# Kernel optimization log

Measured on AMD Instinct MI355X. Metric: run time of the kernel, lower is better.

Reference implementation:

```python
import jax, jax.numpy as jnp
import numpy as np

E, S, D, A, L, H, C = 8, 6000, 128, 16, 64, 256, 64
B = 50            # no_batches hardcoded in torch forward
T = S // B        # number of outer integration steps
DT = 0.5          # solver dt; t_horizon=[0,1] -> 2 reversible-Heun substeps
NSUB = 2
SQDT = float(np.sqrt(DT))


def setup_inputs():
    ks = jax.random.split(jax.random.key(0), 24)
    w = lambda k, shp, s=0.05: (jax.random.normal(k, shp) * s).astype(jnp.float32)
    z = lambda shp: jnp.zeros(shp, jnp.float32)
    return dict(
        xs=w(ks[0], (E, S, D), 1.0),
        actions=w(ks[1], (E, S, A), 1.0),
        z0_noise=w(ks[2], (T, E, B, L), 1.0),
        dW=w(ks[3], (T, NSUB, E * B, L), 1.0),
        enc_w1=w(ks[4], (E, D, H)), enc_b1=z((E, H)),
        enc_w2=w(ks[5], (E, H, C)), enc_b2=z((E, C)),
        qz0_w=w(ks[6], (E, C, 2 * L)), qz0_b=z((E, 2 * L)),
        act_w=w(ks[7], (E, L + A + D, L)), act_b=z((E, L)),
        fw1=w(ks[8], (L, H)), fb1=z((H,)),
        fw2=w(ks[9], (H, H)), fb2=z((H,)),
        fw3=w(ks[10], (H, L)), fb3=z((L,)),
        hw1=w(ks[11], (L, H)), hb1=z((H,)),
        hw2=w(ks[12], (H, H)), hb2=z((H,)),
        hw3=w(ks[13], (H, L)), hb3=z((L,)),
        gw1=w(ks[14], (L, H)), gb1=z((L, H)),
        gw2=w(ks[15], (L, H), 0.02), gb2=jnp.ones((L,), jnp.float32),
        pw1=w(ks[16], (E, L, H)), pb1=z((E, H)),
        pw2=w(ks[17], (E, H, H)), pb2=z((E, H)),
        pw3=w(ks[18], (E, H, D)), pb3=z((E, D)),
        pz0_mean=z((E, 1, L)), pz0_logstd=z((E, 1, L)),
    )


def reference(xs, actions, z0_noise, dW,
              enc_w1, enc_b1, enc_w2, enc_b2, qz0_w, qz0_b, act_w, act_b,
              fw1, fb1, fw2, fb2, fw3, fb3, hw1, hb1, hw2, hb2, hw3, hb3,
              gw1, gb1, gw2, gb2, pw1, pb1, pw2, pb2, pw3, pb3,
              pz0_mean, pz0_logstd):
    xs_r = xs.reshape(E, T, B, D).transpose(1, 0, 2, 3)       # [T,E,B,D]
    act_r = actions.reshape(E, T, B, A).transpose(1, 0, 2, 3)  # [T,E,B,A]

    def mlp3(y, w1, b1, w2, b2, w3, b3):
        h1 = jax.nn.sigmoid(y @ w1 + b1)
        h2 = jax.nn.sigmoid(h1 @ w2 + b2)
        return h2 @ w3 + b3

    def g_fn(y):  # per-latent-dim diagonal diffusion nets, vectorized over L
        hc = jax.nn.sigmoid(y[..., None] * gw1 + gb1)          # [N,L,H]
        return jnp.sum(hc * gw2, axis=-1) + gb2                # [N,L]

    def drift_all(zc):
        fz = mlp3(zc, fw1, fb1, fw2, fb2, fw3, fb3)
        hz = mlp3(zc, hw1, hb1, hw2, hb2, hw3, hb3)
        gz = g_fn(zc)
        u = (fz - hz) / gz
        return fz, gz, 0.5 * jnp.sum(u * u, axis=-1)           # logqp drift

    def sde_solve(zini, dWs):  # reversible Heun, Stratonovich, logqp-augmented
        zc = zh = zini
        lc = lh = jnp.zeros(zini.shape[0], zini.dtype)
        fz, gz, lf = drift_all(zc)
        for k in range(NSUB):
            dWk = dWs[k] * SQDT
            zh_n = 2.0 * zc - zh + fz * DT + gz * dWk
            lh_n = 2.0 * lc - lh + lf * DT
            fz1, gz1, lf1 = drift_all(zh_n)
            zc = zc + 0.5 * (fz + fz1) * DT + 0.5 * (gz + gz1) * dWk
            lc = lc + 0.5 * (lf + lf1) * DT
            zh, lh, fz, gz, lf = zh_n, lh_n, fz1, gz1, lf1
        return zc, lc

    def step(z_prev, inp):
        i, x_i, a_i, n_i, dW_i = inp
        c1 = jax.nn.sigmoid(jnp.einsum('ebd,edh->ebh', x_i, enc_w1) + enc_b1[:, None])
        ctx = jnp.einsum('ebh,ehc->ebc', c1, enc_w2) + enc_b2[:, None]
        q = jnp.einsum('ebc,eck->ebk', ctx, qz0_w) + qz0_b[:, None]
        qm, ql = q[..., :L], q[..., L:]
        z0 = qm + jnp.exp(ql) * n_i
        z_in = jnp.where(i == 0, z0, z_prev)
        lat = jnp.concatenate([z_in, a_i, x_i], axis=-1)
        z_enc = jnp.einsum('ebf,efl->ebl', lat, act_w) + act_b[:, None]
        zf, lr = sde_solve(z_enc.reshape(E * B, L), dW_i)
        z_new = zf.reshape(E, B, L)
        p1 = jax.nn.sigmoid(jnp.einsum('ebl,elh->ebh', z_new, pw1) + pb1[:, None])
        p2 = jax.nn.sigmoid(jnp.einsum('ebh,ehk->ebk', p1, pw2) + pb2[:, None])
        xm = jnp.einsum('ebh,ehd->ebd', p2, pw3) + pb3[:, None]
        # KL(q(z0) || p(z0)) elementwise, p has mean pz0_mean, logstd pz0_logstd
        kl = (pz0_logstd - ql
              + (jnp.exp(2.0 * ql) + (qm - pz0_mean) ** 2) / (2.0 * jnp.exp(2.0 * pz0_logstd))
              - 0.5)
        logqp0 = kl.sum(-1).mean(-1)  # [E]
        return z_new, (xm, lr.reshape(E, B), logqp0)

    z_init = jnp.zeros((E, B, L), xs.dtype)
    _, (xm_all, lr_all, lq0_all) = jax.lax.scan(
        step, z_init, (jnp.arange(T), xs_r, act_r, z0_noise, dW))
    predicted_xs = xm_all.transpose(1, 0, 2, 3).reshape(E, T * B, D)
    logqp_path = lr_all.mean(-1).sum(0) + lq0_all.sum(0)  # [E]
    return logqp_path, predicted_xs
```

## Files before the change

kernel.cpp:

```cpp
#include <hip/hip_runtime.h>
#include <math.h>

#define E 8
#define S 6000
#define D 128
#define A 16
#define L 64
#define H 256
#define C 64
#define B 50
#define T 120
#define NSUB 2
#define FLAT 208
#define RTOT 400
#define RPB 10
#define NBLK (RTOT / RPB)
#define BGRP 10
#define NBG 5

#define DT 0.5f
#define SQDT 0.70710678118654752440f

#define GNT 4096
#define GYMIN (-128.0f)
#define GDY 0.0625f
#define GINVDY 16.0f

typedef __attribute__((ext_vector_type(8))) short bf16x8;
typedef __attribute__((ext_vector_type(4))) float f32x4;

#define MFMA16(a, b, c) __builtin_amdgcn_mfma_f32_16x16x32_bf16(a, b, c, 0, 0, 0)

__device__ __forceinline__ float sigf(float x) {
    return __builtin_amdgcn_rcpf(1.0f + __expf(-x));
}

__device__ __forceinline__ unsigned short f2bf(float x) {
    union { float f; unsigned u; } v; v.f = x;
    return (unsigned short)((v.u + 0x8000u) >> 16);
}

__device__ __forceinline__ void bar_lgkm() {
    asm volatile("s_waitcnt lgkmcnt(0)" ::: "memory");
    __builtin_amdgcn_s_barrier();
}

__global__ void gtab_kernel(const float* __restrict__ gw1, const float* __restrict__ gb1,
                            const float* __restrict__ gw2, const float* __restrict__ gb2,
                            float* __restrict__ tab) {
    int idx = blockIdx.x * blockDim.x + threadIdx.x;
    if (idx >= L * GNT) return;
    int l = idx / GNT, i = idx % GNT;
    float y = GYMIN + (float)i * GDY;
    const float* w1 = gw1 + l * H;
    const float* b1 = gb1 + l * H;
    const float* w2 = gw2 + l * H;
    float acc = gb2[l];
    #pragma unroll 4
    for (int h = 0; h < H; ++h) acc += w2[h] * (1.0f / (1.0f + __expf(-(y * w1[h] + b1[h]))));
    tab[idx] = acc;
}

__global__ void packB_kernel(const float* __restrict__ src, unsigned short* __restrict__ dst,
                             int K, int N) {
    int idx = blockIdx.x * 256 + threadIdx.x;
    if (idx >= K * N) return;
    int j = idx & 7;
    int lane = (idx >> 3) & 63;
    int t2 = idx >> 9;
    int KC = K >> 5;
    int kc = t2 % KC, n = t2 / KC;
    int k = (kc << 5) + ((lane >> 4) << 3) + j;
    int c = (n << 4) + (lane & 15);
    union { float f; unsigned u; } v; v.f = src[k * N + c];
    dst[idx] = (unsigned short)((v.u + 0x7FFFu + ((v.u >> 16) & 1u)) >> 16);
}

__global__ void packAW_kernel(const float* __restrict__ aw, unsigned short* __restrict__ dst) {
    int idx = blockIdx.x * 256 + threadIdx.x;
    if (idx >= E * L * L) return;
    int e = idx >> 12;
    int rem = idx & 4095;
    int j = rem & 7;
    int lane = (rem >> 3) & 63;
    int t2 = rem >> 9;
    int kc = t2 & 1, n = t2 >> 1;
    int k = (kc << 5) + ((lane >> 4) << 3) + j;
    int c = (n << 4) + (lane & 15);
    union { float f; unsigned u; } v; v.f = aw[((size_t)e * FLAT + k) * L + c];
    dst[idx] = (unsigned short)((v.u + 0x7FFFu + ((v.u >> 16) & 1u)) >> 16);
}

__global__ __launch_bounds__(256) void enc_kernel(const float* __restrict__ xs, const float* __restrict__ z0n,
                           const float* __restrict__ ew1, const float* __restrict__ eb1,
                           const float* __restrict__ ew2, const float* __restrict__ eb2,
                           const float* __restrict__ qw,  const float* __restrict__ qb,
                           const float* __restrict__ pm,  const float* __restrict__ pl,
                           float* __restrict__ z0buf, float* __restrict__ logqp0p) {
    int bid = blockIdx.x;
    int bg = bid % NBG; int te = bid / NBG; int e = te % E; int t = te / E;
    int tid = threadIdx.x;
    __shared__ float xsh[BGRP][D];
    __shared__ float c1s[BGRP][H];
    __shared__ float part[4][C][BGRP];
    __shared__ float ctxs[BGRP][C];
    __shared__ float qs[BGRP][2 * L];

    for (int i = tid; i < BGRP * D; i += 256) {
        int j = i / D, d = i % D;
        xsh[j][d] = xs[((size_t)e * S + (size_t)t * B + bg * BGRP + j) * D + d];
    }
    __syncthreads();
    {
        float bias = eb1[e * H + tid];
        float acc[BGRP];
        #pragma unroll
        for (int j = 0; j < BGRP; ++j) acc[j] = bias;
        const float* w = ew1 + (size_t)e * D * H + tid;
        #pragma unroll 4
        for (int d = 0; d < D; ++d) {
            float wv = w[(size_t)d * H];
            #pragma unroll
            for (int j = 0; j < BGRP; ++j) acc[j] += xsh[j][d] * wv;
        }
        #pragma unroll
        for (int j = 0; j < BGRP; ++j) c1s[j][tid] = sigf(acc[j]);
    }
    __syncthreads();
    {
        int c = tid & 63, kq = tid >> 6;
        float acc[BGRP];
        #pragma unroll
        for (int j = 0; j < BGRP; ++j) acc[j] = 0.f;
        const float* w = ew2 + (size_t)e * H * C + c;
        #pragma unroll 4
        for (int h = kq * 64; h < kq * 64 + 64; ++h) {
            float wv = w[(size_t)h * C];
            #pragma unroll
            for (int j = 0; j < BGRP; ++j) acc[j] += c1s[j][h] * wv;
        }
        #pragma unroll
        for (int j = 0; j < BGRP; ++j) part[kq][c][j] = acc[j];
    }
    __syncthreads();
    if (tid < C) {
        float bias = eb2[e * C + tid];
        #pragma unroll
        for (int j = 0; j < BGRP; ++j)
            ctxs[j][tid] = part[0][tid][j] + part[1][tid][j] + part[2][tid][j] + part[3][tid][j] + bias;
    }
    __syncthreads();
    if (tid < 2 * L) {
        float bias = qb[e * 2 * L + tid];
        float acc[BGRP];
        #pragma unroll
        for (int j = 0; j < BGRP; ++j) acc[j] = bias;
        const float* w = qw + (size_t)e * C * 2 * L + tid;
        #pragma unroll 4
        for (int c = 0; c < C; ++c) {
            float wv = w[(size_t)c * 2 * L];
            #pragma unroll
            for (int j = 0; j < BGRP; ++j) acc[j] += ctxs[j][c] * wv;
        }
        #pragma unroll
        for (int j = 0; j < BGRP; ++j) qs[j][tid] = acc[j];
    }
    __syncthreads();
    if (tid < L) {
        int l = tid;
        float kacc = 0.f;
        float m = pm[e * L + l], ls = pl[e * L + l];
        float inv2e = 1.0f / (2.0f * __expf(2.0f * ls));
        #pragma unroll
        for (int j = 0; j < BGRP; ++j) {
            float qm = qs[j][l], ql = qs[j][L + l];
            if (t == 0) {
                int b = bg * BGRP + j;
                float n = z0n[((size_t)e * B + b) * L + l];
                z0buf[((size_t)e * B + b) * L + l] = qm + __expf(ql) * n;
            }
            float dq = qm - m;
            kacc += ls - ql + (__expf(2.f * ql) + dq * dq) * inv2e - 0.5f;
        }
        #pragma unroll
        for (int off = 32; off; off >>= 1) kacc += __shfl_xor(kacc, off);
        if (l == 0) logqp0p[bid] = kacc / (float)B;
    }
}

__global__ __launch_bounds__(64) void ax_kernel(const float* __restrict__ xs, const float* __restrict__ actions,
                          const float* __restrict__ aw, const float* __restrict__ ab,
                          float* __restrict__ ax) {
    int bid = blockIdx.x;
    int bg = bid % NBG; int te = bid / NBG; int e = te % E; int t = te / E;
    int tid = threadIdx.x;
    __shared__ float xrow[BGRP][D];
    __shared__ float arow[BGRP][A];
    for (int i = tid; i < BGRP * D; i += 64) {
        int j = i / D, d = i % D;
        xrow[j][d] = xs[((size_t)e * S + (size_t)t * B + bg * BGRP + j) * D + d];
    }
    for (int i = tid; i < BGRP * A; i += 64) {
        int j = i / A, a = i % A;
        arow[j][a] = actions[((size_t)e * S + (size_t)t * B + bg * BGRP + j) * A + a];
    }
    __syncthreads();
    int l = tid;
    float acc[BGRP];
    float bias = ab[e * L + l];
    #pragma unroll
    for (int j = 0; j < BGRP; ++j) acc[j] = bias;
    const float* awp = aw + ((size_t)e * FLAT + L) * L + l;
    #pragma unroll 4
    for (int a = 0; a < A; ++a) {
        float wv = awp[(size_t)a * L];
        #pragma unroll
        for (int j = 0; j < BGRP; ++j) acc[j] += arow[j][a] * wv;
    }
    const float* xwp = aw + ((size_t)e * FLAT + L + A) * L + l;
    #pragma unroll 4
    for (int d = 0; d < D; ++d) {
        float wv = xwp[(size_t)d * L];
        #pragma unroll
        for (int j = 0; j < BGRP; ++j) acc[j] += xrow[j][d] * wv;
    }
    size_t rbase = (size_t)t * RTOT + e * B + bg * BGRP;
    #pragma unroll
    for (int j = 0; j < BGRP; ++j) ax[(rbase + j) * L + l] = acc[j];
}

__global__ __launch_bounds__(512, 2) void seq_kernel(
    const unsigned short* __restrict__ pkAW, const float* __restrict__ dW,
    const float* __restrict__ z0buf, const float* __restrict__ axbuf,
    const unsigned short* __restrict__ pk1, const unsigned short* __restrict__ pk2,
    const unsigned short* __restrict__ pk3,
    const float* __restrict__ fb1, const float* __restrict__ hb1,
    const float* __restrict__ fb2, const float* __restrict__ hb2,
    const float* __restrict__ fb3, const float* __restrict__ hb3,
    const float* __restrict__ gtab, float* __restrict__ z_all, float* __restrict__ rowlr)
{
    __shared__ __align__(16) bf16x8 w1L[4096];
    __shared__ __align__(16) unsigned short ybfA[1024];
    __shared__ __align__(16) unsigned short ybfZ[1024];
    __shared__ __align__(16) unsigned short o1[2][4096];
    __shared__ __align__(16) unsigned short o2[2][4096];
    __shared__ float fh2[2][16][64];
    __shared__ float zcS[16][64];
    __shared__ float axS[RPB * L];

    int tid = threadIdx.x;
    int wv = tid >> 6;
    int lane = tid & 63;
    int rA = lane & 15, kg = lane >> 4;
    int sw = (rA & 7) << 3;
    int r_base = blockIdx.x * RPB;
    int e = blockIdx.x / 5;

    for (int i = tid; i < 4096; i += 512) w1L[i] = ((const bf16x8*)pk1)[i];

    int net = wv >> 2;
    int nq  = wv & 3;
    int na  = nq << 2;
    int n0c = nq;
    int lZ = (nq << 4) + rA;

    bf16x8 W0r0 = {}, W0r1 = {}, W2r[32], W3r[8];
    if (wv < 4) {
        const bf16x8* p0 = (const bf16x8*)pkAW + (e << 9);
        W0r0 = p0[(nq * 2 + 0) * 64 + lane];
        W0r1 = p0[(nq * 2 + 1) * 64 + lane];
    }
    {
        const bf16x8* p2 = (const bf16x8*)pk2 + net * 8192;
        #pragma unroll
        for (int i2 = 0; i2 < 4; ++i2)
            #pragma unroll
            for (int kc = 0; kc < 8; ++kc)
                W2r[i2 * 8 + kc] = p2[((na + i2) * 8 + kc) * 64 + lane];
        const bf16x8* p3 = (const bf16x8*)pk3 + net * 2048;
        #pragma unroll
        for (int kc = 0; kc < 8; ++kc)
            W3r[kc] = p3[(n0c * 8 + kc) * 64 + lane];
    }
    float biasA[4], biasB[4], biasC;
    {
        const float* b1 = net ? hb1 : fb1;
        const float* b2 = net ? hb2 : fb2;
        const float* b3 = net ? hb3 : fb3;
        #pragma unroll
        for (int i2 = 0; i2 < 4; ++i2) {
            biasA[i2] = b1[((na + i2) << 4) + rA];
            biasB[i2] = b2[((na + i2) << 4) + rA];
        }
        biasC = b3[(n0c << 4) + rA];
    }

    int orowA = tid >> 6, olA = tid & 63;
    bool ownB = (tid < RPB * L - 512);
    int orowB = 8 + (tid >> 6);
    float zcA = 0.f, zhA_ = 0.f, fzA = 0.f, gzA = 1.f, dwAA = 0.f, dwBA = 0.f;
    float gtA0 = 1.f, gtA1 = 1.f, gfrA = 0.f, scalA = 0.f;
    float zcB = 0.f, zhB_ = 0.f, fzB = 0.f, gzB = 1.f, dwAB = 0.f, dwBB = 0.f;
    float gtB0 = 1.f, gtB1 = 1.f, gfrB = 0.f, scalB = 0.f;

    for (int i = tid; i < 1024; i += 512) {
        int r = i >> 6;
        float v = (i < RPB * L) ? z0buf[(size_t)r_base * L + i] : 0.f;
        ybfZ[i ^ ((r & 7) << 3)] = f2bf(v);
    }
    axS[tid] = axbuf[((size_t)0 * RTOT + r_base) * L + tid];
    if (ownB) axS[512 + tid] = axbuf[((size_t)0 * RTOT + r_base) * L + 512 + tid];
    __syncthreads();

    auto gprepA = [&](float v) {
        float x = (v - GYMIN) * GINVDY;
        x = fminf(fmaxf(x, 0.0f), (float)(GNT - 2) + 0.999f);
        int ii = (int)x;
        gfrA = x - (float)ii;
        const float* tl = gtab + ((size_t)olA << 12);
        gtA0 = tl[ii];
        gtA1 = tl[ii + 1];
    };
    auto gprepB = [&](float v) {
        float x = (v - GYMIN) * GINVDY;
        x = fminf(fmaxf(x, 0.0f), (float)(GNT - 2) + 0.999f);
        int ii = (int)x;
        gfrB = x - (float)ii;
        const float* tl = gtab + ((size_t)olA << 12);
        gtB0 = tl[ii];
        gtB1 = tl[ii + 1];
    };

    for (int t = 0; t < T; ++t) {
        if (wv < 4) {
            bf16x8 Z0 = *(const bf16x8*)&ybfZ[((rA << 6) + (kg << 3)) ^ sw];
            bf16x8 Z1 = *(const bf16x8*)&ybfZ[((rA << 6) + 32 + (kg << 3)) ^ sw];
            f32x4 acc = (f32x4){0.f, 0.f, 0.f, 0.f};
            acc = MFMA16(Z0, W0r0, acc);
            acc = MFMA16(Z1, W0r1, acc);
            #pragma unroll
            for (int rr = 0; rr < 4; ++rr) {
                int r = (kg << 2) + rr;
                float axv = (r < RPB) ? axS[(r << 6) + lZ] : 0.f;
                float v = acc[rr] + axv;
                zcS[r][lZ] = v;
                ybfA[((r << 6) + lZ) ^ ((r & 7) << 3)] = f2bf(v);
            }
        }
        bar_lgkm();

        #pragma clang loop unroll(disable)
        for (int d = 0; d < 3; ++d) {
            if (d == 0) {
                zcA = zcS[orowA][olA];
                zhA_ = zcA;
                gprepA(zcA);
                dwAA = dW[((size_t)(2 * t) * RTOT + r_base) * L + tid] * SQDT;
                dwBA = dW[((size_t)(2 * t + 1) * RTOT + r_base) * L + tid] * SQDT;
                int tn = (t + 1 < T) ? t + 1 : t;
                axS[tid] = axbuf[((size_t)tn * RTOT + r_base) * L + tid];
                if (ownB) {
                    zcB = zcS[orowB][olA];
                    zhB_ = zcB;
                    gprepB(zcB);
                    dwAB = dW[((size_t)(2 * t) * RTOT + r_base) * L + 512 + tid] * SQDT;
                    dwBB = dW[((size_t)(2 * t + 1) * RTOT + r_base) * L + 512 + tid] * SQDT;
                    axS[512 + tid] = axbuf[((size_t)tn * RTOT + r_base) * L + 512 + tid];
                }
            }
            {
                bf16x8 A0 = *(const bf16x8*)&ybfA[((rA << 6) + (kg << 3)) ^ sw];
                bf16x8 A1 = *(const bf16x8*)&ybfA[((rA << 6) + 32 + (kg << 3)) ^ sw];
                f32x4 acc[4];
                #pragma unroll
                for (int i2 = 0; i2 < 4; ++i2) {
                    acc[i2] = (f32x4){biasA[i2], biasA[i2], biasA[i2], biasA[i2]};
                    acc[i2] = MFMA16(A0, w1L[net * 2048 + ((na + i2) * 2 + 0) * 64 + lane], acc[i2]);
                    acc[i2] = MFMA16(A1, w1L[net * 2048 + ((na + i2) * 2 + 1) * 64 + lane], acc[i2]);
                }
                unsigned short* o1n = o1[net];
                #pragma unroll
                for (int i2 = 0; i2 < 4; ++i2) {
                    int c = ((na + i2) << 4) + rA;
                    #pragma unroll
                    for (int rr = 0; rr < 4; ++rr) {
                        int r = (kg << 2) + rr;
                        o1n[((r << 8) + c) ^ ((r & 7) << 3)] = f2bf(sigf(acc[i2][rr]));
                    }
                }
            }
            bar_lgkm();
            {
                const unsigned short* o1n = o1[net];
                f32x4 acc[4];
                #pragma unroll
                for (int i2 = 0; i2 < 4; ++i2)
                    acc[i2] = (f32x4){biasB[i2], biasB[i2], biasB[i2], biasB[i2]};
                #pragma unroll
                for (int kc = 0; kc < 8; ++kc) {
                    bf16x8 Ak = *(const bf16x8*)&o1n[((rA << 8) + (kc << 5) + (kg << 3)) ^ sw];
                    #pragma unroll
                    for (int i2 = 0; i2 < 4; ++i2)
                        acc[i2] = MFMA16(Ak, W2r[i2 * 8 + kc], acc[i2]);
                }
                unsigned short* o2n = o2[net];
                #pragma unroll
                for (int i2 = 0; i2 < 4; ++i2) {
                    int c = ((na + i2) << 4) + rA;
                    #pragma unroll
                    for (int rr = 0; rr < 4; ++rr) {
                        int r = (kg << 2) + rr;
                        o2n[((r << 8) + c) ^ ((r & 7) << 3)] = f2bf(sigf(acc[i2][rr]));
                    }
                }
            }
            bar_lgkm();
            {
                const unsigned short* o2n = o2[net];
                f32x4 acc = (f32x4){biasC, biasC, biasC, biasC};
                f32x4 accb = (f32x4){0.f, 0.f, 0.f, 0.f};
                #pragma unroll
                for (int kc = 0; kc < 4; ++kc) {
                    bf16x8 Ak0 = *(const bf16x8*)&o2n[((rA << 8) + ((2 * kc) << 5) + (kg << 3)) ^ sw];
                    bf16x8 Ak1 = *(const bf16x8*)&o2n[((rA << 8) + ((2 * kc + 1) << 5) + (kg << 3)) ^ sw];
                    acc  = MFMA16(Ak0, W3r[2 * kc], acc);
                    accb = MFMA16(Ak1, W3r[2 * kc + 1], accb);
                }
                int c = (n0c << 4) + rA;
                #pragma unroll
                for (int rr = 0; rr < 4; ++rr)
                    fh2[net][(kg << 2) + rr][c] = acc[rr] + accb[rr];
            }
            bar_lgkm();
            {
                float fvA = fh2[0][orowA][olA];
                float hvA = fh2[1][orowA][olA];
                float gvA = gtA0 * (1.0f - gfrA) + gtA1 * gfrA;
                float uA = (fvA - hvA) / gvA;
                float usA = uA * uA;
                float fvB = 0.f, hvB = 0.f, gvB = 1.f, usB = 0.f;
                if (ownB) {
                    fvB = fh2[0][orowB][olA];
                    hvB = fh2[1][orowB][olA];
                    gvB = gtB0 * (1.0f - gfrB) + gtB1 * gfrB;
                    float uB = (fvB - hvB) / gvB;
                    usB = uB * uB;
                }
                if (d == 0) {
                    scalA += usA; fzA = fvA; gzA = gvA;
                    float y1 = zcA + fvA * DT + gvA * dwAA;
                    zhA_ = y1;
                    ybfA[tid ^ ((orowA & 7) << 3)] = f2bf(y1);
                    gprepA(y1);
                    if (ownB) {
                        scalB += usB; fzB = fvB; gzB = gvB;
                        float y1b = zcB + fvB * DT + gvB * dwAB;
                        zhB_ = y1b;
                        ybfA[(512 + tid) ^ ((orowB & 7) << 3)] = f2bf(y1b);
                        gprepB(y1b);
                    }
                } else if (d == 1) {
                    zcA += 0.5f * (fzA + fvA) * DT + 0.5f * (gzA + gvA) * dwAA;
                    scalA += 2.0f * usA;
                    float y2 = 2.f * zcA - zhA_ + fvA * DT + gvA * dwBA;
                    fzA = fvA; gzA = gvA;
                    ybfA[tid ^ ((orowA & 7) << 3)] = f2bf(y2);
                    gprepA(y2);
                    if (ownB) {
                        zcB += 0.5f * (fzB + fvB) * DT + 0.5f * (gzB + gvB) * dwAB;
                        scalB += 2.0f * usB;
                        float y2b = 2.f * zcB - zhB_ + fvB * DT + gvB * dwBB;
                        fzB = fvB; gzB = gvB;
                        ybfA[(512 + tid) ^ ((orowB & 7) << 3)] = f2bf(y2b);
                        gprepB(y2b);
                    }
                } else {
                    zcA += 0.5f * (fzA + fvA) * DT + 0.5f * (gzA + gvA) * dwBA;
                    scalA += usA;
                    z_all[((size_t)t * RTOT + r_base) * L + tid] = zcA;
                    ybfZ[tid ^ ((orowA & 7) << 3)] = f2bf(zcA);
                    if (ownB) {
                        zcB += 0.5f * (fzB + fvB) * DT + 0.5f * (gzB + gvB) * dwBB;
                        scalB += usB;
                        z_all[((size_t)t * RTOT + r_base) * L + 512 + tid] = zcB;
                        ybfZ[(512 + tid) ^ ((orowB & 7) << 3)] = f2bf(zcB);
                    }
                }
            }
            bar_lgkm();
        }
    }
    {
        float s = scalA;
        #pragma unroll
        for (int off = 32; off; off >>= 1) s += __shfl_xor(s, off);
        if (olA == 0) rowlr[r_base + orowA] = 0.25f * DT * s;
        float sb = ownB ? scalB : 0.f;
        #pragma unroll
        for (int off = 32; off; off >>= 1) sb += __shfl_xor(sb, off);
        if (ownB && olA == 0) rowlr[r_base + orowB] = 0.25f * DT * sb;
    }
}

__global__ __launch_bounds__(256) void proj_kernel(const float* __restrict__ z_all,
                            const float* __restrict__ pw1, const float* __restrict__ pb1,
                            const float* __restrict__ pw2, const float* __restrict__ pb2,
                            const float* __restrict__ pw3, const float* __restrict__ pb3,
                            float* __restrict__ out) {
    int bid = blockIdx.x;
    int bg = bid % NBG; int te = bid / NBG; int e = te % E; int t = te / E;
    int tid = threadIdx.x;
    __shared__ float zs[BGRP][L];
    __shared__ float p1s[BGRP][H];
    __shared__ float p2s[BGRP][H];
    __shared__ float part3[D][BGRP];
    size_t rbase = (size_t)t * RTOT + e * B + bg * BGRP;
    for (int i = tid; i < BGRP * L; i += 256) {
        int j = i >> 6, ll = i & 63;
        zs[j][ll] = z_all[(rbase + j) * L + ll];
    }
    __syncthreads();
    {
        float bias = pb1[e * H + tid];
        float acc[BGRP];
        #pragma unroll
        for (int j = 0; j < BGRP; ++j) acc[j] = bias;
        const float* w = pw1 + (size_t)e * L * H + tid;
        #pragma unroll 4
        for (int k = 0; k < L; ++k) {
            float wv = w[(size_t)k * H];
            #pragma unroll
            for (int j = 0; j < BGRP; ++j) acc[j] += zs[j][k] * wv;
        }
        #pragma unroll
        for (int j = 0; j < BGRP; ++j) p1s[j][tid] = sigf(acc[j]);
    }
    __syncthreads();
    {
        float bias = pb2[e * H + tid];
        float acc[BGRP];
        #pragma unroll
        for (int j = 0; j < BGRP; ++j) acc[j] = bias;
        const float* w = pw2 + (size_t)e * H * H + tid;
        #pragma unroll 4
        for (int k = 0; k < H; ++k) {
            float wv = w[(size_t)k * H];
            #pragma unroll
            for (int j = 0; j < BGRP; ++j) acc[j] += p1s[j][k] * wv;
        }
        #pragma unroll
        for (int j = 0; j < BGRP; ++j) p2s[j][tid] = sigf(acc[j]);
    }
    __syncthreads();
    float acc3[BGRP];
    {
        int dd = tid & 127, kh = tid >> 7;
        #pragma unroll
        for (int j = 0; j < BGRP; ++j) acc3[j] = 0.f;
        const float* w = pw3 + (size_t)e * H * D + dd;
        #pragma unroll 4
        for (int k = kh * 128; k < kh * 128 + 128; ++k) {
            float wv = w[(size_t)k * D];
            #pragma unroll
            for (int j = 0; j < BGRP; ++j) acc3[j] += p2s[j][k] * wv;
        }
        if (kh == 1) {
            #pragma unroll
            for (int j = 0; j < BGRP; ++j) part3[dd][j] = acc3[j];
        }
    }
    __syncthreads();
    if (tid < D) {
        float bias = pb3[e * D + tid];
        #pragma unroll
        for (int j = 0; j < BGRP; ++j) {
            out[8 + ((size_t)e * S + (size_t)t * B + bg * BGRP + j) * D + tid]
                = acc3[j] + part3[tid][j] + bias;
        }
    }
}

__global__ void fin_kernel(const float* __restrict__ logqp0p, const float* __restrict__ rowlr,
                           float* __restrict__ out) {
    int e = threadIdx.x;
    if (e < E) {
        float acc = 0.f;
        for (int t = 0; t < T; ++t)
            for (int bg = 0; bg < NBG; ++bg)
                acc += logqp0p[(t * E + e) * NBG + bg];
        float s = 0.f;
        for (int b = 0; b < B; ++b) s += rowlr[e * B + b];
        out[e] = acc + s / (float)B;
    }
}

extern "C" void kernel_launch(void* const* d_in, const int* in_sizes, int n_in,
                              void* d_out, int out_size, void* d_ws, size_t ws_size,
                              hipStream_t stream) {
    const float* xs      = (const float*)d_in[0];
    const float* actions = (const float*)d_in[1];
    const float* z0n     = (const float*)d_in[2];
    const float* dWp     = (const float*)d_in[3];
    const float* ew1     = (const float*)d_in[4];
    const float* eb1     = (const float*)d_in[5];
    const float* ew2     = (const float*)d_in[6];
    const float* eb2     = (const float*)d_in[7];
    const float* qw      = (const float*)d_in[8];
    const float* qb      = (const float*)d_in[9];
    const float* aw      = (const float*)d_in[10];
    const float* ab      = (const float*)d_in[11];
    const float* fw1     = (const float*)d_in[12];
    const float* fb1     = (const float*)d_in[13];
    const float* fw2     = (const float*)d_in[14];
    const float* fb2     = (const float*)d_in[15];
    const float* fw3     = (const float*)d_in[16];
    const float* fb3     = (const float*)d_in[17];
    const float* hw1     = (const float*)d_in[18];
    const float* hb1     = (const float*)d_in[19];
    const float* hw2     = (const float*)d_in[20];
    const float* hb2     = (const float*)d_in[21];
    const float* hw3     = (const float*)d_in[22];
    const float* hb3     = (const float*)d_in[23];
    const float* gw1     = (const float*)d_in[24];
    const float* gb1     = (const float*)d_in[25];
    const float* gw2     = (const float*)d_in[26];
    const float* gb2     = (const float*)d_in[27];
    const float* pw1     = (const float*)d_in[28];
    const float* pb1     = (const float*)d_in[29];
    const float* pw2     = (const float*)d_in[30];
    const float* pb2     = (const float*)d_in[31];
    const float* pw3     = (const float*)d_in[32];
    const float* pb3     = (const float*)d_in[33];
    const float* pm      = (const float*)d_in[34];
    const float* pl      = (const float*)d_in[35];

    float* ws      = (float*)d_ws;
    float* z0buf   = ws;
    float* axbuf   = z0buf + 25600;
    float* z_all   = axbuf + 3072000;
    float* logqp0p = z_all + 3072000;
    float* rowlr   = logqp0p + 4800;
    float* gtab    = rowlr + 400;
    unsigned short* pku = (unsigned short*)(gtab + 262144);
    unsigned short* pk1 = pku;
    unsigned short* pk2 = pk1 + 32768;
    unsigned short* pk3 = pk2 + 131072;
    unsigned short* pkAW = pk3 + 32768;
    float* out     = (float*)d_out;

    packB_kernel<<<64,  256, 0, stream>>>(fw1, pk1,          64, 256);
    packB_kernel<<<64,  256, 0, stream>>>(hw1, pk1 + 16384,  64, 256);
    packB_kernel<<<256, 256, 0, stream>>>(fw2, pk2,          256, 256);
    packB_kernel<<<256, 256, 0, stream>>>(hw2, pk2 + 65536,  256, 256);
    packB_kernel<<<64,  256, 0, stream>>>(fw3, pk3,          256, 64);
    packB_kernel<<<64,  256, 0, stream>>>(hw3, pk3 + 16384,  256, 64);
    packAW_kernel<<<128, 256, 0, stream>>>(aw, pkAW);
    gtab_kernel<<<1024, 256, 0, stream>>>(gw1, gb1, gw2, gb2, gtab);
    enc_kernel<<<T * E * NBG, 256, 0, stream>>>(xs, z0n, ew1, eb1, ew2, eb2, qw, qb, pm, pl, z0buf, logqp0p);
    ax_kernel<<<T * E * NBG, 64, 0, stream>>>(xs, actions, aw, ab, axbuf);
    seq_kernel<<<NBLK, 512, 0, stream>>>(pkAW, dWp, z0buf, axbuf,
                                         pk1, pk2, pk3,
                                         fb1, hb1, fb2, hb2, fb3, hb3,
                                         gtab, z_all, rowlr);
    proj_kernel<<<T * E * NBG, 256, 0, stream>>>(z_all, pw1, pb1, pw2, pb2, pw3, pb3, out);
    fin_kernel<<<1, 64, 0, stream>>>(logqp0p, rowlr, out);
}
```

Measured before the change: 2.617 ms.

## Fuse output MLP layer and SDE update into four waves, dropping a barrier

New measurement: 3.462 ms. 32.3% more time.

```diff
diff --git a/kernel.cpp b/kernel.cpp
--- a/kernel.cpp
+++ b/kernel.cpp
@@ -240,13 +240,13 @@
     const float* __restrict__ gtab, float* __restrict__ z_all, float* __restrict__ rowlr)
 {
     __shared__ __align__(16) bf16x8 w1L[4096];
+    __shared__ __align__(16) bf16x8 w0L[512];
+    __shared__ __align__(16) bf16x8 fw3L[2048];
     __shared__ __align__(16) unsigned short ybfA[1024];
     __shared__ __align__(16) unsigned short ybfZ[1024];
     __shared__ __align__(16) unsigned short o1[2][4096];
     __shared__ __align__(16) unsigned short o2[2][4096];
-    __shared__ float fh2[2][16][64];
-    __shared__ float zcS[16][64];
-    __shared__ float axS[RPB * L];
+    __shared__ float scalS[16][64];
 
     int tid = threadIdx.x;
     int wv = tid >> 6;
@@ -257,19 +257,14 @@
     int e = blockIdx.x / 5;
 
     for (int i = tid; i < 4096; i += 512) w1L[i] = ((const bf16x8*)pk1)[i];
+    w0L[tid] = ((const bf16x8*)pkAW)[(e << 9) + tid];
+    for (int i = tid; i < 2048; i += 512) fw3L[i] = ((const bf16x8*)pk3)[i];
 
     int net = wv >> 2;
     int nq  = wv & 3;
     int na  = nq << 2;
-    int n0c = nq;
-    int lZ = (nq << 4) + rA;
-
-    bf16x8 W0r0 = {}, W0r1 = {}, W2r[32], W3r[8];
-    if (wv < 4) {
-        const bf16x8* p0 = (const bf16x8*)pkAW + (e << 9);
-        W0r0 = p0[(nq * 2 + 0) * 64 + lane];
-        W0r1 = p0[(nq * 2 + 1) * 64 + lane];
-    }
+
+    bf16x8 W2r[32], hW3r[8];
     {
         const bf16x8* p2 = (const bf16x8*)pk2 + net * 8192;
         #pragma unroll
@@ -277,97 +272,63 @@
             #pragma unroll
             for (int kc = 0; kc < 8; ++kc)
                 W2r[i2 * 8 + kc] = p2[((na + i2) * 8 + kc) * 64 + lane];
-        const bf16x8* p3 = (const bf16x8*)pk3 + net * 2048;
+        const bf16x8* p3h = (const bf16x8*)pk3 + 2048;
         #pragma unroll
         for (int kc = 0; kc < 8; ++kc)
-            W3r[kc] = p3[(n0c * 8 + kc) * 64 + lane];
-    }
-    float biasA[4], biasB[4], biasC;
+            hW3r[kc] = p3h[(nq * 8 + kc) * 64 + lane];
+    }
+    float biasA[4], biasB[4];
     {
         const float* b1 = net ? hb1 : fb1;
         const float* b2 = net ? hb2 : fb2;
-        const float* b3 = net ? hb3 : fb3;
         #pragma unroll
         for (int i2 = 0; i2 < 4; ++i2) {
             biasA[i2] = b1[((na + i2) << 4) + rA];
             biasB[i2] = b2[((na + i2) << 4) + rA];
         }
-        biasC = b3[(n0c << 4) + rA];
-    }
-
-    int orowA = tid >> 6, olA = tid & 63;
-    bool ownB = (tid < RPB * L - 512);
-    int orowB = 8 + (tid >> 6);
-    float zcA = 0.f, zhA_ = 0.f, fzA = 0.f, gzA = 1.f, dwAA = 0.f, dwBA = 0.f;
-    float gtA0 = 1.f, gtA1 = 1.f, gfrA = 0.f, scalA = 0.f;
-    float zcB = 0.f, zhB_ = 0.f, fzB = 0.f, gzB = 1.f, dwAB = 0.f, dwBB = 0.f;
-    float gtB0 = 1.f, gtB1 = 1.f, gfrB = 0.f, scalB = 0.f;
+    }
+    int cc = (nq << 4) + rA;
+    float biasCf = fb3[cc], biasCh = hb3[cc];
+
+    float zc[4], zh[4], fz[4], gz[4], yv[4], scal[4], dwA[4], dwB[4];
+    #pragma unroll
+    for (int i = 0; i < 4; ++i) { zc[i]=0.f; zh[i]=0.f; fz[i]=0.f; gz[i]=1.f; yv[i]=0.f; scal[i]=0.f; dwA[i]=0.f; dwB[i]=0.f; }
 
     for (int i = tid; i < 1024; i += 512) {
         int r = i >> 6;
         float v = (i < RPB * L) ? z0buf[(size_t)r_base * L + i] : 0.f;
         ybfZ[i ^ ((r & 7) << 3)] = f2bf(v);
     }
-    axS[tid] = axbuf[((size_t)0 * RTOT + r_base) * L + tid];
-    if (ownB) axS[512 + tid] = axbuf[((size_t)0 * RTOT + r_base) * L + 512 + tid];
-    __syncthreads();
-
-    auto gprepA = [&](float v) {
-        float x = (v - GYMIN) * GINVDY;
-        x = fminf(fmaxf(x, 0.0f), (float)(GNT - 2) + 0.999f);
-        int ii = (int)x;
-        gfrA = x - (float)ii;
-        const float* tl = gtab + ((size_t)olA << 12);
-        gtA0 = tl[ii];
-        gtA1 = tl[ii + 1];
-    };
-    auto gprepB = [&](float v) {
-        float x = (v - GYMIN) * GINVDY;
-        x = fminf(fmaxf(x, 0.0f), (float)(GNT - 2) + 0.999f);
-        int ii = (int)x;
-        gfrB = x - (float)ii;
-        const float* tl = gtab + ((size_t)olA << 12);
-        gtB0 = tl[ii];
-        gtB1 = tl[ii + 1];
-    };
+    __syncthreads();
 
     for (int t = 0; t < T; ++t) {
         if (wv < 4) {
+            float axv[4];
+            #pragma unroll
+            for (int i = 0; i < 4; ++i) {
+                int r = (kg << 2) + i;
+                bool real = (r < RPB);
+                axv[i] = real ? axbuf[((size_t)t * RTOT + r_base + r) * L + cc] : 0.f;
+                dwA[i] = real ? dW[((size_t)(2 * t) * RTOT + r_base + r) * L + cc] * SQDT : 0.f;
+                dwB[i] = real ? dW[((size_t)(2 * t + 1) * RTOT + r_base + r) * L + cc] * SQDT : 0.f;
+            }
             bf16x8 Z0 = *(const bf16x8*)&ybfZ[((rA << 6) + (kg << 3)) ^ sw];
             bf16x8 Z1 = *(const bf16x8*)&ybfZ[((rA << 6) + 32 + (kg << 3)) ^ sw];
             f32x4 acc = (f32x4){0.f, 0.f, 0.f, 0.f};
-            acc = MFMA16(Z0, W0r0, acc);
-            acc = MFMA16(Z1, W0r1, acc);
-            #pragma unroll
-            for (int rr = 0; rr < 4; ++rr) {
-                int r = (kg << 2) + rr;
-                float axv = (r < RPB) ? axS[(r << 6) + lZ] : 0.f;
-                float v = acc[rr] + axv;
-                zcS[r][lZ] = v;
-                ybfA[((r << 6) + lZ) ^ ((r & 7) << 3)] = f2bf(v);
+            acc = MFMA16(Z0, w0L[(nq * 2 + 0) * 64 + lane], acc);
+            acc = MFMA16(Z1, w0L[(nq * 2 + 1) * 64 + lane], acc);
+            #pragma unroll
+            for (int i = 0; i < 4; ++i) {
+                int r = (kg << 2) + i;
+                float v = acc[i] + axv[i];
+                zc[i] = v; zh[i] = v; yv[i] = v;
+                ybfA[((r << 6) + cc) ^ ((r & 7) << 3)] = f2bf(v);
             }
         }
         bar_lgkm();
 
         #pragma clang loop unroll(disable)
         for (int d = 0; d < 3; ++d) {
-            if (d == 0) {
-                zcA = zcS[orowA][olA];
-                zhA_ = zcA;
-                gprepA(zcA);
-                dwAA = dW[((size_t)(2 * t) * RTOT + r_base) * L + tid] * SQDT;
-                dwBA = dW[((size_t)(2 * t + 1) * RTOT + r_base) * L + tid] * SQDT;
-                int tn = (t + 1 < T) ? t + 1 : t;
-                axS[tid] = axbuf[((size_t)tn * RTOT + r_base) * L + tid];
-                if (ownB) {
-                    zcB = zcS[orowB][olA];
-                    zhB_ = zcB;
-                    gprepB(zcB);
-                    dwAB = dW[((size_t)(2 * t) * RTOT + r_base) * L + 512 + tid] * SQDT;
-                    dwBB = dW[((size_t)(2 * t + 1) * RTOT + r_base) * L + 512 + tid] * SQDT;
-                    axS[512 + tid] = axbuf[((size_t)tn * RTOT + r_base) * L + 512 + tid];
-                }
-            }
             {
                 bf16x8 A0 = *(const bf16x8*)&ybfA[((rA << 6) + (kg << 3)) ^ sw];
                 bf16x8 A1 = *(const bf16x8*)&ybfA[((rA << 6) + 32 + (kg << 3)) ^ sw];
@@ -415,90 +376,79 @@
                 }
             }
             bar_lgkm();
-            {
-                const unsigned short* o2n = o2[net];
-                f32x4 acc = (f32x4){biasC, biasC, biasC, biasC};
-                f32x4 accb = (f32x4){0.f, 0.f, 0.f, 0.f};
+            if (wv < 4) {
+                float gt0[4], gt1[4], gfr[4];
+                const float* tl = gtab + ((size_t)cc << 12);
+                #pragma unroll
+                for (int i = 0; i < 4; ++i) {
+                    float x = (yv[i] - GYMIN) * GINVDY;
+                    x = fminf(fmaxf(x, 0.0f), (float)(GNT - 2) + 0.999f);
+                    int ii = (int)x;
+                    gfr[i] = x - (float)ii;
+                    gt0[i] = tl[ii];
+                    gt1[i] = tl[ii + 1];
+                }
+                const unsigned short* o2f = o2[0];
+                const unsigned short* o2h = o2[1];
+                f32x4 aF = (f32x4){biasCf, biasCf, biasCf, biasCf};
+                f32x4 bF = (f32x4){0.f, 0.f, 0.f, 0.f};
+                f32x4 aH = (f32x4){biasCh, biasCh, biasCh, biasCh};
+                f32x4 bH = (f32x4){0.f, 0.f, 0.f, 0.f};
                 #pragma unroll
                 for (int kc = 0; kc < 4; ++kc) {
-                    bf16x8 Ak0 = *(const bf16x8*)&o2n[((rA << 8) + ((2 * kc) << 5) + (kg << 3)) ^ sw];
-                    bf16x8 Ak1 = *(const bf16x8*)&o2n[((rA << 8) + ((2 * kc + 1) << 5) + (kg << 3)) ^ sw];
-                    acc  = MFMA16(Ak0, W3r[2 * kc], acc);
-                    accb = MFMA16(Ak1, W3r[2 * kc + 1], accb);
+                    bf16x8 Af0 = *(const bf16x8*)&o2f[((rA << 8) + ((2*kc) << 5) + (kg << 3)) ^ sw];
+                    bf16x8 Af1 = *(const bf16x8*)&o2f[((rA << 8) + ((2*kc+1) << 5) + (kg << 3)) ^ sw];
+                    aF = MFMA16(Af0, fw3L[(nq * 8 + 2*kc) * 64 + lane], aF);
+                    bF = MFMA16(Af1, fw3L[(nq * 8 + 2*kc+1) * 64 + lane], bF);
+                    bf16x8 Ah0 = *(const bf16x8*)&o2h[((rA << 8) + ((2*kc) << 5) + (kg << 3)) ^ sw];
+                    bf16x8 Ah1 = *(const bf16x8*)&o2h[((rA << 8) + ((2*kc+1) << 5) + (kg << 3)) ^ sw];
+                    aH = MFMA16(Ah0, hW3r[2*kc], aH);
+                    bH = MFMA16(Ah1, hW3r[2*kc+1], bH);
                 }
-                int c = (n0c << 4) + rA;
-                #pragma unroll
-                for (int rr = 0; rr < 4; ++rr)
-                    fh2[net][(kg << 2) + rr][c] = acc[rr] + accb[rr];
-            }
-            bar_lgkm();
-            {
-                float fvA = fh2[0][orowA][olA];
-                float hvA = fh2[1][orowA][olA];
-                float gvA = gtA0 * (1.0f - gfrA) + gtA1 * gfrA;
-                float uA = (fvA - hvA) / gvA;
-                float usA = uA * uA;
-                float fvB = 0.f, hvB = 0.f, gvB = 1.f, usB = 0.f;
-                if (ownB) {
-                    fvB = fh2[0][orowB][olA];
-                    hvB = fh2[1][orowB][olA];
-                    gvB = gtB0 * (1.0f - gfrB) + gtB1 * gfrB;
-                    float uB = (fvB - hvB) / gvB;
-                    usB = uB * uB;
-                }
-                if (d == 0) {
-                    scalA += usA; fzA = fvA; gzA = gvA;
-                    float y1 = zcA + fvA * DT + gvA * dwAA;
-                    zhA_ = y1;
-                    ybfA[tid ^ ((orowA & 7) << 3)] = f2bf(y1);
-                    gprepA(y1);
-                    if (ownB) {
-                        scalB += usB; fzB = fvB; gzB = gvB;
-                        float y1b = zcB + fvB * DT + gvB * dwAB;
-                        zhB_ = y1b;
-                        ybfA[(512 + tid) ^ ((orowB & 7) << 3)] = f2bf(y1b);
-                        gprepB(y1b);
-                    }
-                } else if (d == 1) {
-                    zcA += 0.5f * (fzA + fvA) * DT + 0.5f * (gzA + gvA) * dwAA;
-                    scalA += 2.0f * usA;
-                    float y2 = 2.f * zcA - zhA_ + fvA * DT + gvA * dwBA;
-                    fzA = fvA; gzA = gvA;
-                    ybfA[tid ^ ((orowA & 7) << 3)] = f2bf(y2);
-                    gprepA(y2);
-                    if (ownB) {
-                        zcB += 0.5f * (fzB + fvB) * DT + 0.5f * (gzB + gvB) * dwAB;
-                        scalB += 2.0f * usB;
-                        float y2b = 2.f * zcB - zhB_ + fvB * DT + gvB * dwBB;
-                        fzB = fvB; gzB = gvB;
-                        ybfA[(512 + tid) ^ ((orowB & 7) << 3)] = f2bf(y2b);
-                        gprepB(y2b);
-                    }
-                } else {
-                    zcA += 0.5f * (fzA + fvA) * DT + 0.5f * (gzA + gvA) * dwBA;
-                    scalA += usA;
-                    z_all[((size_t)t * RTOT + r_base) * L + tid] = zcA;
-                    ybfZ[tid ^ ((orowA & 7) << 3)] = f2bf(zcA);
-                    if (ownB) {
-                        zcB += 0.5f * (fzB + fvB) * DT + 0.5f * (gzB + gvB) * dwBB;
-                        scalB += usB;
-                        z_all[((size_t)t * RTOT + r_base) * L + 512 + tid] = zcB;
-                        ybfZ[(512 + tid) ^ ((orowB & 7) << 3)] = f2bf(zcB);
+                #pragma unroll
+                for (int i = 0; i < 4; ++i) {
+                    int r = (kg << 2) + i;
+                    float fv = aF[i] + bF[i];
+                    float hv = aH[i] + bH[i];
+                    float gv = gt0[i] * (1.0f - gfr[i]) + gt1[i] * gfr[i];
+                    float uu = (fv - hv) / gv;
+                    float us = uu * uu;
+                    if (d == 0) {
+                        scal[i] += us;
+                        fz[i] = fv; gz[i] = gv;
+                        float y1 = zc[i] + fv * DT + gv * dwA[i];
+                        zh[i] = y1; yv[i] = y1;
+                        ybfA[((r << 6) + cc) ^ ((r & 7) << 3)] = f2bf(y1);
+                    } else if (d == 1) {
+                        zc[i] += 0.5f * (fz[i] + fv) * DT + 0.5f * (gz[i] + gv) * dwA[i];
+                        scal[i] += 2.0f * us;
+                        float y2 = 2.f * zc[i] - zh[i] + fv * DT + gv * dwB[i];
+                        fz[i] = fv; gz[i] = gv; yv[i] = y2;
+                        ybfA[((r << 6) + cc) ^ ((r & 7) << 3)] = f2bf(y2);
+                    } else {
+                        zc[i] += 0.5f * (fz[i] + fv) * DT + 0.5f * (gz[i] + gv) * dwB[i];
+                        scal[i] += us;
+                        if (r < RPB) {
+                            z_all[((size_t)t * RTOT + r_base + r) * L + cc] = zc[i];
+                            ybfZ[((r << 6) + cc) ^ ((r & 7) << 3)] = f2bf(zc[i]);
+                        }
                     }
                 }
             }
             bar_lgkm();
         }
     }
-    {
-        float s = scalA;
+    if (wv < 4) {
+        #pragma unroll
+        for (int i = 0; i < 4; ++i)
+            scalS[(kg << 2) + i][cc] = scal[i];
+    }
+    __syncthreads();
+    for (int rr = wv; rr < RPB; rr += 8) {
+        float s = scalS[rr][lane];
         #pragma unroll
         for (int off = 32; off; off >>= 1) s += __shfl_xor(s, off);
-        if (olA == 0) rowlr[r_base + orowA] = 0.25f * DT * s;
-        float sb = ownB ? scalB : 0.f;
-        #pragma unroll
-        for (int off = 32; off; off >>= 1) sb += __shfl_xor(sb, off);
-        if (ownB && olA == 0) rowlr[r_base + orowB] = 0.25f * DT * sb;
+        if (lane == 0) rowlr[r_base + rr] = 0.25f * DT * s;
     }
 }
 
```
